# Performance work log

Measured on AMD Instinct MI355X. Metric: run time of the kernel, lower is better.

The kernel has to match this reference:

```python
import jax, jax.numpy as jnp
import numpy as np

GROUP_SIZE = 128


def _unpack_int4(packed):
    # packed: [..., P] int32, each holding 8 int4 nibbles (LSB-first).
    u = jax.lax.bitcast_convert_type(packed, jnp.uint32)
    shifts = jnp.arange(8, dtype=jnp.uint32) * 4  # nibble bit offsets
    vals = (u[..., None] >> shifts) & jnp.uint32(15)  # [..., P, 8]
    return vals.reshape(*packed.shape[:-1], -1)  # [..., P*8] in [0, 15]


def setup_inputs() -> dict:
    key = jax.random.key(0)
    k1, k2, k3, k4 = jax.random.split(key, 4)
    B, S, K, O = 4, 16, 4096, 11008
    G = K // GROUP_SIZE          # 32 groups
    GP = (G + 7) // 8            # 4 packed-zero columns
    imax = np.iinfo(np.int32).max
    x = jax.random.normal(k1, (B, S, K), dtype=jnp.float16)
    qweight_i32 = jax.random.randint(k2, (O, K // 8), 0, imax, dtype=jnp.int32)
    qzeros_i32 = jax.random.randint(k3, (O, GP), 0, imax, dtype=jnp.int32)
    scales_f16 = jax.random.uniform(k4, (O, G), dtype=jnp.float16,
                                    minval=0.001, maxval=0.02)
    return {"x": x, "qweight_i32": qweight_i32, "qzeros_i32": qzeros_i32,
            "scales_f16": scales_f16}


def reference(x, qweight_i32, qzeros_i32, scales_f16):
    O, G = scales_f16.shape
    K = G * GROUP_SIZE
    # Dequantize: w = (q - z) * s, per-group int4 quantization.
    q = _unpack_int4(qweight_i32)[:, :K].astype(jnp.float16)       # [O, K]
    z = _unpack_int4(qzeros_i32)[:, :G].astype(jnp.float16)        # [O, G]
    z_k = jnp.repeat(z, GROUP_SIZE, axis=1)                        # [O, K]
    s_k = jnp.repeat(scales_f16, GROUP_SIZE, axis=1)               # [O, K]
    w = (q - z_k) * s_k                                            # fp16 [O, K]
    x2d = x.reshape(-1, K).astype(jnp.float16)                     # [m, K]
    out = jnp.matmul(x2d, w.T).astype(jnp.float32)                 # [m, O]
    return out.reshape(*x.shape[:-1], O)
```

## Files before the change

### kernel.cpp

```cpp
#include <hip/hip_runtime.h>
#include <stdint.h>

typedef _Float16 half8  __attribute__((ext_vector_type(8)));
typedef float    floatx4 __attribute__((ext_vector_type(4)));
typedef uint32_t uint4v  __attribute__((ext_vector_type(4)));

#define KDIM 4096
#define ODIM 11008
#define NG   32

__device__ __forceinline__ uint32_t pk_f16(float a, float b) {
    return __builtin_bit_cast(uint32_t, __builtin_amdgcn_cvt_pkrtz(a, b));
}

__global__ __launch_bounds__(256) void cvt_x_kernel(
    const float4* __restrict__ x, uint4v* __restrict__ xh2,
    float* __restrict__ xsumT)
{
    const int i = blockIdx.x * 256 + threadIdx.x;
    const float4 f0 = x[2 * i];
    const float4 f1 = x[2 * i + 1];
    const uint4v v = {pk_f16(f0.x, f1.x), pk_f16(f0.y, f1.y),
                      pk_f16(f0.z, f1.z), pk_f16(f0.w, f1.w)};
    const int m  = i >> 9, c = i & 511;
    const int g  = c >> 4, cg = c & 15, q = cg >> 2, ks = cg & 3;
    const int mt = m >> 4, ml = m & 15;
    xh2[((size_t)(g * 4 + ks) * 4 + mt) * 64 + q * 16 + ml] = v;

    float p = f0.x + f0.y + f0.z + f0.w + f1.x + f1.y + f1.z + f1.w;
    p += __shfl_xor(p, 1);
    p += __shfl_xor(p, 2);
    p += __shfl_xor(p, 4);
    p += __shfl_xor(p, 8);
    if ((threadIdx.x & 15) == 0) xsumT[g * 64 + m] = p;
}

__global__ __launch_bounds__(256, 2) void w4a16_kernel(
    const uint4v*   __restrict__ xh2,
    const uint4v*   __restrict__ qw,
    const uint32_t* __restrict__ qz,
    const float*    __restrict__ sc,
    const float*    __restrict__ xsumT,
    float*          __restrict__ out)
{
    __shared__ float red[4][16][64];

    const int t    = threadIdx.x;
    const int kw   = t >> 6;
    const int lane = t & 63;
    const int q    = lane >> 4;
    const int ml   = lane & 15;

    const int o0 = blockIdx.x * 16;
    const int o  = o0 + ml;
    const int g0 = kw * 8;

    const uint4v* qwp = qw + (size_t)o * 128 + g0 * 4 + q;
    const uint32_t zdw = qz[(size_t)o * 4 + kw];
    const floatx4 sv0 = *reinterpret_cast<const floatx4*>(sc + (size_t)o * NG + g0);
    const floatx4 sv1 = *reinterpret_cast<const floatx4*>(sc + (size_t)o * NG + g0 + 4);

    const uint4v* xp = xh2 + (size_t)g0 * 1024 + lane;
    const float*  xs = xsumT + (size_t)g0 * 64 + q * 4;

    floatx4 acc[4] = {{0.f,0.f,0.f,0.f},{0.f,0.f,0.f,0.f},
                      {0.f,0.f,0.f,0.f},{0.f,0.f,0.f,0.f}};

    uint4v ubuf[2];
    ubuf[0] = qwp[0];
    ubuf[1] = qwp[4];

    #pragma unroll 1
    for (int gl = 0; gl < 8; ++gl) {
        const uint4v ucur = ubuf[gl & 1];
        if (gl + 2 < 8) ubuf[gl & 1] = qwp[(gl + 2) * 4];

        const uint32_t zn  = (zdw >> (gl * 4)) & 0xFu;
        const float    s   = (gl < 4) ? sv0[gl] : sv1[gl - 4];
        const float    czs = s * (1024.0f + (float)zn);

        floatx4 tmp[4] = {{0.f,0.f,0.f,0.f},{0.f,0.f,0.f,0.f},
                          {0.f,0.f,0.f,0.f},{0.f,0.f,0.f,0.f}};

        #pragma unroll
        for (int h = 0; h < 2; ++h) {
            uint4v ax[8];
            #pragma unroll
            for (int i = 0; i < 8; ++i)
                ax[i] = xp[(size_t)(gl * 16 + h * 8 + i) * 64];

            #pragma unroll
            for (int k2 = 0; k2 < 2; ++k2) {
                const int ks = h * 2 + k2;
                const uint32_t ud = ucur[ks];
                const uint4v bw = {
                    ( ud         & 0x000F000Fu) | 0x64006400u,
                    ((ud >> 4)   & 0x000F000Fu) | 0x64006400u,
                    ((ud >> 8)   & 0x000F000Fu) | 0x64006400u,
                    ((ud >> 12)  & 0x000F000Fu) | 0x64006400u};
                const half8 b = __builtin_bit_cast(half8, bw);
                #pragma unroll
                for (int mt = 0; mt < 4; ++mt)
                    tmp[mt] = __builtin_amdgcn_mfma_f32_16x16x32_f16(
                        __builtin_bit_cast(half8, ax[k2 * 4 + mt]), b, tmp[mt],
                        0, 0, 0);
            }
        }

        #pragma unroll
        for (int mt = 0; mt < 4; ++mt) {
            const floatx4 xg = *reinterpret_cast<const floatx4*>(
                xs + gl * 64 + mt * 16);
            #pragma unroll
            for (int r = 0; r < 4; ++r)
                acc[mt][r] += s * tmp[mt][r] - czs * xg[r];
        }
    }

    #pragma unroll
    for (int mt = 0; mt < 4; ++mt)
        #pragma unroll
        for (int r = 0; r < 4; ++r)
            red[kw][mt * 4 + r][lane] = acc[mt][r];
    __syncthreads();

    const int mt2 = t >> 6;
    #pragma unroll
    for (int r = 0; r < 4; ++r) {
        const int i = mt2 * 4 + r;
        const float sum = red[0][i][lane] + red[1][i][lane]
                        + red[2][i][lane] + red[3][i][lane];
        out[(size_t)(mt2 * 16 + q * 4 + r) * ODIM + o] = sum;
    }
}

extern "C" void kernel_launch(void* const* d_in, const int* in_sizes, int n_in,
                              void* d_out, int out_size, void* d_ws, size_t ws_size,
                              hipStream_t stream) {
    const float*    x       = (const float*)d_in[0];
    const uint32_t* qweight = (const uint32_t*)d_in[1];
    const uint32_t* qzeros  = (const uint32_t*)d_in[2];
    const float*    scales  = (const float*)d_in[3];
    float* out = (float*)d_out;

    uint4v* xh2   = (uint4v*)d_ws;
    float*  xsumT = (float*)((char*)d_ws + 512 * 1024);

    cvt_x_kernel<<<dim3(128), dim3(256), 0, stream>>>((const float4*)x, xh2, xsumT);
    w4a16_kernel<<<dim3(ODIM / 16), dim3(256), 0, stream>>>(
        xh2, (const uint4v*)qweight, qzeros, scales, xsumT, out);
}
```

Baseline: 94.48 us.

## Process two 16-column output tiles per block to reuse activation fragments

Each block now computes 32 output columns instead of 16, so every activation fragment loaded from global memory feeds two MFMA chains (one per weight tile). This halves activation traffic per output and halves the grid size (344 blocks instead of 688). The costs are more registers per thread, which may hurt occupancy under launch_bounds(256,2), and fewer blocks to spread across the CUs, plus doubled shared memory for the reduction.

```diff
diff --git a/kernel.cpp b/kernel.cpp
--- a/kernel.cpp
+++ b/kernel.cpp
@@ -43,7 +43,7 @@
     const float*    __restrict__ xsumT,
     float*          __restrict__ out)
 {
-    __shared__ float red[4][16][64];
+    __shared__ float red[4][2][16][64];
 
     const int t    = threadIdx.x;
     const int kw   = t >> 6;
@@ -51,36 +51,52 @@
     const int q    = lane >> 4;
     const int ml   = lane & 15;
 
-    const int o0 = blockIdx.x * 16;
-    const int o  = o0 + ml;
+    const int o0 = blockIdx.x * 32;
+    const int oa = o0 + ml;
+    const int ob = o0 + 16 + ml;
     const int g0 = kw * 8;
 
-    const uint4v* qwp = qw + (size_t)o * 128 + g0 * 4 + q;
-    const uint32_t zdw = qz[(size_t)o * 4 + kw];
-    const floatx4 sv0 = *reinterpret_cast<const floatx4*>(sc + (size_t)o * NG + g0);
-    const floatx4 sv1 = *reinterpret_cast<const floatx4*>(sc + (size_t)o * NG + g0 + 4);
+    const uint4v* qwpa = qw + (size_t)oa * 128 + g0 * 4 + q;
+    const uint4v* qwpb = qw + (size_t)ob * 128 + g0 * 4 + q;
+    const uint32_t zdwa = qz[(size_t)oa * 4 + kw];
+    const uint32_t zdwb = qz[(size_t)ob * 4 + kw];
+    const floatx4 sva0 = *reinterpret_cast<const floatx4*>(sc + (size_t)oa * NG + g0);
+    const floatx4 sva1 = *reinterpret_cast<const floatx4*>(sc + (size_t)oa * NG + g0 + 4);
+    const floatx4 svb0 = *reinterpret_cast<const floatx4*>(sc + (size_t)ob * NG + g0);
+    const floatx4 svb1 = *reinterpret_cast<const floatx4*>(sc + (size_t)ob * NG + g0 + 4);
 
     const uint4v* xp = xh2 + (size_t)g0 * 1024 + lane;
     const float*  xs = xsumT + (size_t)g0 * 64 + q * 4;
 
-    floatx4 acc[4] = {{0.f,0.f,0.f,0.f},{0.f,0.f,0.f,0.f},
-                      {0.f,0.f,0.f,0.f},{0.f,0.f,0.f,0.f}};
+    floatx4 accA[4] = {{0.f,0.f,0.f,0.f},{0.f,0.f,0.f,0.f},
+                       {0.f,0.f,0.f,0.f},{0.f,0.f,0.f,0.f}};
+    floatx4 accB[4] = {{0.f,0.f,0.f,0.f},{0.f,0.f,0.f,0.f},
+                       {0.f,0.f,0.f,0.f},{0.f,0.f,0.f,0.f}};
 
-    uint4v ubuf[2];
-    ubuf[0] = qwp[0];
-    ubuf[1] = qwp[4];
+    uint4v ubufA[2], ubufB[2];
+    ubufA[0] = qwpa[0];  ubufB[0] = qwpb[0];
+    ubufA[1] = qwpa[4];  ubufB[1] = qwpb[4];
 
     #pragma unroll 1
     for (int gl = 0; gl < 8; ++gl) {
-        const uint4v ucur = ubuf[gl & 1];
-        if (gl + 2 < 8) ubuf[gl & 1] = qwp[(gl + 2) * 4];
+        const uint4v ucA = ubufA[gl & 1];
+        const uint4v ucB = ubufB[gl & 1];
+        if (gl + 2 < 8) {
+            ubufA[gl & 1] = qwpa[(gl + 2) * 4];
+            ubufB[gl & 1] = qwpb[(gl + 2) * 4];
+        }
 
-        const uint32_t zn  = (zdw >> (gl * 4)) & 0xFu;
-        const float    s   = (gl < 4) ? sv0[gl] : sv1[gl - 4];
-        const float    czs = s * (1024.0f + (float)zn);
+        const uint32_t zna = (zdwa >> (gl * 4)) & 0xFu;
+        const uint32_t znb = (zdwb >> (gl * 4)) & 0xFu;
+        const float    sa  = (gl < 4) ? sva0[gl] : sva1[gl - 4];
+        const float    sb  = (gl < 4) ? svb0[gl] : svb1[gl - 4];
+        const float    czsa = sa * (1024.0f + (float)zna);
+        const float    czsb = sb * (1024.0f + (float)znb);
 
-        floatx4 tmp[4] = {{0.f,0.f,0.f,0.f},{0.f,0.f,0.f,0.f},
-                          {0.f,0.f,0.f,0.f},{0.f,0.f,0.f,0.f}};
+        floatx4 tA[4] = {{0.f,0.f,0.f,0.f},{0.f,0.f,0.f,0.f},
+                         {0.f,0.f,0.f,0.f},{0.f,0.f,0.f,0.f}};
+        floatx4 tB[4] = {{0.f,0.f,0.f,0.f},{0.f,0.f,0.f,0.f},
+                         {0.f,0.f,0.f,0.f},{0.f,0.f,0.f,0.f}};
 
         #pragma unroll
         for (int h = 0; h < 2; ++h) {
@@ -92,18 +108,28 @@
             #pragma unroll
             for (int k2 = 0; k2 < 2; ++k2) {
                 const int ks = h * 2 + k2;
-                const uint32_t ud = ucur[ks];
-                const uint4v bw = {
-                    ( ud         & 0x000F000Fu) | 0x64006400u,
-                    ((ud >> 4)   & 0x000F000Fu) | 0x64006400u,
-                    ((ud >> 8)   & 0x000F000Fu) | 0x64006400u,
-                    ((ud >> 12)  & 0x000F000Fu) | 0x64006400u};
-                const half8 b = __builtin_bit_cast(half8, bw);
+                const uint32_t udA = ucA[ks];
+                const uint32_t udB = ucB[ks];
+                const uint4v bwA = {
+                    ( udA         & 0x000F000Fu) | 0x64006400u,
+                    ((udA >> 4)   & 0x000F000Fu) | 0x64006400u,
+                    ((udA >> 8)   & 0x000F000Fu) | 0x64006400u,
+                    ((udA >> 12)  & 0x000F000Fu) | 0x64006400u};
+                const uint4v bwB = {
+                    ( udB         & 0x000F000Fu) | 0x64006400u,
+                    ((udB >> 4)   & 0x000F000Fu) | 0x64006400u,
+                    ((udB >> 8)   & 0x000F000Fu) | 0x64006400u,
+                    ((udB >> 12)  & 0x000F000Fu) | 0x64006400u};
+                const half8 bA = __builtin_bit_cast(half8, bwA);
+                const half8 bB = __builtin_bit_cast(half8, bwB);
                 #pragma unroll
-                for (int mt = 0; mt < 4; ++mt)
-                    tmp[mt] = __builtin_amdgcn_mfma_f32_16x16x32_f16(
-                        __builtin_bit_cast(half8, ax[k2 * 4 + mt]), b, tmp[mt],
-                        0, 0, 0);
+                for (int mt = 0; mt < 4; ++mt) {
+                    const half8 a = __builtin_bit_cast(half8, ax[k2 * 4 + mt]);
+                    tA[mt] = __builtin_amdgcn_mfma_f32_16x16x32_f16(
+                        a, bA, tA[mt], 0, 0, 0);
+                    tB[mt] = __builtin_amdgcn_mfma_f32_16x16x32_f16(
+                        a, bB, tB[mt], 0, 0, 0);
+                }
             }
         }
 
@@ -112,26 +138,32 @@
             const floatx4 xg = *reinterpret_cast<const floatx4*>(
                 xs + gl * 64 + mt * 16);
             #pragma unroll
-            for (int r = 0; r < 4; ++r)
-                acc[mt][r] += s * tmp[mt][r] - czs * xg[r];
+            for (int r = 0; r < 4; ++r) {
+                accA[mt][r] += sa * tA[mt][r] - czsa * xg[r];
+                accB[mt][r] += sb * tB[mt][r] - czsb * xg[r];
+            }
         }
     }
 
     #pragma unroll
     for (int mt = 0; mt < 4; ++mt)
         #pragma unroll
-        for (int r = 0; r < 4; ++r)
-            red[kw][mt * 4 + r][lane] = acc[mt][r];
+        for (int r = 0; r < 4; ++r) {
+            red[kw][0][mt * 4 + r][lane] = accA[mt][r];
+            red[kw][1][mt * 4 + r][lane] = accB[mt][r];
+        }
     __syncthreads();
 
     const int mt2 = t >> 6;
     #pragma unroll
-    for (int r = 0; r < 4; ++r) {
-        const int i = mt2 * 4 + r;
-        const float sum = red[0][i][lane] + red[1][i][lane]
-                        + red[2][i][lane] + red[3][i][lane];
-        out[(size_t)(mt2 * 16 + q * 4 + r) * ODIM + o] = sum;
-    }
+    for (int oc = 0; oc < 2; ++oc)
+        #pragma unroll
+        for (int r = 0; r < 4; ++r) {
+            const int i = mt2 * 4 + r;
+            const float sum = red[0][oc][i][lane] + red[1][oc][i][lane]
+                            + red[2][oc][i][lane] + red[3][oc][i][lane];
+            out[(size_t)(mt2 * 16 + q * 4 + r) * ODIM + o0 + oc * 16 + ml] = sum;
+        }
 }
 
 extern "C" void kernel_launch(void* const* d_in, const int* in_sizes, int n_in,
@@ -147,6 +179,6 @@
     float*  xsumT = (float*)((char*)d_ws + 512 * 1024);
 
     cvt_x_kernel<<<dim3(128), dim3(256), 0, stream>>>((const float4*)x, xh2, xsumT);
-    w4a16_kernel<<<dim3(ODIM / 16), dim3(256), 0, stream>>>(
+    w4a16_kernel<<<dim3(ODIM / 32), dim3(256), 0, stream>>>(
         xh2, (const uint4v*)qweight, qzeros, scales, xsumT, out);
 }
```

After: 93.88 us. No clear change (-0.6%).
